# Kernel optimization log

Measured on AMD Instinct MI355X. Metric: run time of the kernel, lower is better.

The kernel has to match this reference:

```python
import jax, jax.numpy as jnp
import numpy as np
from jax import lax

NUM_SKETCH = 3
BN_EPS = 1e-5


def setup_inputs() -> dict:
    key = jax.random.key(0)
    ks = jax.random.split(key, 8)
    B, C, H, W = 32, 128, 64, 64
    D = C // 4  # comp_rate = 4
    k = 3
    x = jax.random.normal(ks[0], (B, C, H, W), dtype=jnp.float32)
    fan = C * k * k
    w1 = jax.random.normal(ks[1], (C, C, k, k), dtype=jnp.float32) / np.sqrt(fan)
    w2 = jax.random.normal(ks[2], (C, C, k, k), dtype=jnp.float32) / np.sqrt(fan)
    gamma1 = jnp.ones((C,), jnp.float32); beta1 = jnp.zeros((C,), jnp.float32)
    gamma2 = jnp.ones((C,), jnp.float32); beta2 = jnp.zeros((C,), jnp.float32)
    # count-sketch hash matrices: hs[j] is (D, C), each column c has a single 1
    idx = jax.random.randint(ks[3], (NUM_SKETCH, C), 0, D)
    hs = jax.nn.one_hot(idx, D, dtype=jnp.float32).transpose(0, 2, 1)  # (3, D, C)
    ss = (jax.random.randint(ks[4], (NUM_SKETCH, C), 0, 2) * 2 - 1).astype(jnp.float32)  # (3, C) signs
    return {"x": x, "w1": w1, "w2": w2, "gamma1": gamma1, "beta1": beta1,
            "gamma2": gamma2, "beta2": beta2, "hs": hs, "ss": ss}


def _sketch_conv_unsketch(x, w, hs, ss):
    # w: (Co, Ci, k, k); hs: (J, D, Co); ss: (J, Co)
    Co, Ci, k, _ = w.shape
    J, D, _ = hs.shape
    B, _, H, W = x.shape
    wf = w.reshape(Co, -1)  # (Co, M)
    # sketched weights per sketch j: h_j @ (wf * s_j[:, None])
    w_sk = jnp.einsum('jdc,jc,cm->jdm', hs, ss, wf).reshape(J * D, Ci, k, k)
    # one conv with J*D output channels (padding=1, stride=1 hardcoded in source)
    y = lax.conv_general_dilated(x, w_sk, window_strides=(1, 1),
                                 padding=[(1, 1), (1, 1)],
                                 dimension_numbers=('NCHW', 'OIHW', 'NCHW'))
    y = y.reshape(B, J, D, H, W)
    # unsketch activations: h_j^T @ y_j, then sign scale (num_s=1 so inner median is identity)
    y_un = jnp.einsum('jdc,bjdhw->jbchw', hs, y) * ss[:, None, :, None, None]
    return jnp.median(y_un, axis=0)  # median over the 3 sketches -> (B, Co, H, W)


def _bn_relu(y, gamma, beta):
    # BatchNorm2d in training mode: biased batch stats over (N, H, W)
    mean = jnp.mean(y, axis=(0, 2, 3), keepdims=True)
    var = jnp.var(y, axis=(0, 2, 3), keepdims=True)
    yhat = (y - mean) * lax.rsqrt(var + BN_EPS)
    return jax.nn.relu(yhat * gamma[None, :, None, None] + beta[None, :, None, None])


def reference(x, w1, w2, gamma1, beta1, gamma2, beta2, hs, ss):
    residual = x
    out1 = _bn_relu(_sketch_conv_unsketch(x, w1, hs, ss), gamma1, beta1)
    del out1  # faithful to source bug: second conv loop uses x, discarding out1
    out = _bn_relu(_sketch_conv_unsketch(x, w2, hs, ss), gamma2, beta2)
    return out + residual
```

## Files before the change

### kernel.cpp

```cpp
#include <hip/hip_runtime.h>
#include <stdint.h>

typedef __bf16 bf16x8 __attribute__((ext_vector_type(8)));
typedef float  f32x4  __attribute__((ext_vector_type(4)));

static constexpr int Bn = 32, Cn = 128, Hn = 64, Wn = 64, HWn = 4096;
static constexpr size_t OFF_XT    = 0;
static constexpr size_t OFF_WF    = 33554432;
static constexpr size_t OFF_IDX   = 33775616;
static constexpr size_t OFF_M     = 33777152;
static constexpr size_t OFF_STATS = 67331584;
static constexpr size_t OFF_ZERO  = 67347968;

__device__ __forceinline__ unsigned short f32_to_bf16(float f) {
    union { float f; unsigned u; } v; v.f = f;
    unsigned u = v.u;
    return (unsigned short)((u + 0x7FFFu + ((u >> 16) & 1u)) >> 16);
}
__device__ __forceinline__ float bf16_to_f32(unsigned short h) {
    union { unsigned u; float f; } v; v.u = ((unsigned)h) << 16;
    return v.f;
}
__device__ __forceinline__ float bf_lo(unsigned w) {
    union { unsigned u; float f; } v; v.u = w << 16; return v.f;
}
__device__ __forceinline__ float bf_hi(unsigned w) {
    union { unsigned u; float f; } v; v.u = w & 0xffff0000u; return v.f;
}
__device__ __forceinline__ float med3(float z0, float z1, float z2) {
    float lo = fminf(z0, z1), hi = fmaxf(z0, z1);
    return fmaxf(lo, fminf(hi, z2));
}
__device__ __forceinline__ void gload_lds16(const unsigned short* g, unsigned short* l) {
    __builtin_amdgcn_global_load_lds(
        (const __attribute__((address_space(1))) unsigned int*)(const void*)g,
        (__attribute__((address_space(3))) unsigned int*)(void*)l,
        16, 0, 0);
}

__global__ __launch_bounds__(256) void k_prep(const float* __restrict__ x,
                                              unsigned short* __restrict__ xT,
                                              const float* __restrict__ w2,
                                              const float* __restrict__ hs,
                                              const float* __restrict__ ss,
                                              unsigned short* __restrict__ wf,
                                              int* __restrict__ idx,
                                              float* __restrict__ stats16,
                                              float* __restrict__ zerop) {
    __shared__ __align__(16) unsigned char smraw[20480];
    int t = threadIdx.x;
    if (blockIdx.x < 432) {
        int*   idxs = (int*)smraw;
        float* sss  = (float*)(smraw + 1536);
        for (int i = t; i < 384; i += 256) {
            int j = i >> 7, c = i & 127;
            int found = 0;
#pragma unroll
            for (int d = 0; d < 32; ++d)
                if (hs[(j * 32 + d) * 128 + c] > 0.5f) found = d;
            idxs[i] = found;
            sss[i]  = ss[i];
        }
        __syncthreads();
        int f = blockIdx.x * 256 + t;
        int jj   = f & 7;
        int lane = (f >> 3) & 63;
        int nt   = (f >> 9) % 6;
        int qt   = f / (512 * 6);
        int tp   = qt % 9;
        int q    = qt / 9;
        int k  = ((lane >> 4) << 3) + jj;
        int ci = q * 32 + k;
        int n  = nt * 16 + (lane & 15);
        int j = n >> 5, d = n & 31;
        const int*   ij = idxs + j * 128;
        const float* sj = sss  + j * 128;
        float sum = 0.f;
        for (int c = 0; c < 128; ++c)
            if (ij[c] == d) sum += sj[c] * w2[(c * 128 + ci) * 9 + tp];
        wf[f] = f32_to_bf16(sum);
    } else if (blockIdx.x == 432) {
        for (int i = t; i < 384; i += 256) {
            int j = i >> 7, c = i & 127;
            int found = 0;
            for (int d = 0; d < 32; ++d)
                if (hs[(j * 32 + d) * 128 + c] > 0.5f) found = d;
            idx[i] = found;
        }
        for (int i = t; i < 4096; i += 256) stats16[i] = 0.f;
        if (t < 32) zerop[t] = 0.f;
    } else {
        unsigned short* sm = (unsigned short*)smraw;
        int blk = blockIdx.x - 433;
        int pt = blk & 15, q = (blk >> 4) & 3, b = blk >> 6;
        int p0 = pt * 256;
        const float* xp = x + ((size_t)(b * Cn + q * 32) * HWn) + p0 + t;
#pragma unroll
        for (int cil = 0; cil < 32; ++cil)
            sm[t * 40 + cil] = f32_to_bf16(xp[(size_t)cil * HWn]);
        __syncthreads();
        uint4* dst = (uint4*)(xT + ((size_t)(b * 4 + q) * HWn + p0) * 32);
#pragma unroll
        for (int pass = 0; pass < 4; ++pass) {
            int pix = pass * 64 + (t >> 2);
            int ch  = t & 3;
            dst[pix * 4 + ch] = *(const uint4*)(&sm[pix * 40 + ch * 8]);
        }
    }
}

__global__ __launch_bounds__(256, 2) void k_conv(const unsigned short* __restrict__ xT,
                                                 const unsigned short* __restrict__ wf,
                                                 const int* __restrict__ idx,
                                                 const float* __restrict__ ss,
                                                 unsigned short* __restrict__ m_out,
                                                 float* __restrict__ stats16,
                                                 const unsigned short* __restrict__ zerop) {
    __shared__ __align__(16) unsigned short sm[25344];
    int tid  = threadIdx.x;
    int blk  = blockIdx.x;
    int tile = blk & 15, b = blk >> 4;
    int ty0  = tile * 4;
    int wv   = tid >> 6, lane = tid & 63;
    int quad = lane >> 4, l15 = lane & 15;

    unsigned short* priv = sm + wv * 6336;

    f32x4 acc[4][6];
#pragma unroll
    for (int a = 0; a < 4; ++a)
#pragma unroll
        for (int nb = 0; nb < 6; ++nb) acc[a][nb] = (f32x4){0.f, 0.f, 0.f, 0.f};

    const unsigned short* wl = wf + lane * 8;

#define STAGE_W(qv)                                                                   \
    {                                                                                 \
        const unsigned short* xq = xT + (size_t)(b * 4 + (qv)) * (HWn * 32);          \
        _Pragma("unroll")                                                             \
        for (int i = 0; i < 13; ++i) {                                                \
            if (i < 12 || lane < 24) {                                                \
                int k  = i * 64 + lane;                                               \
                int r  = k >> 2;                                                      \
                int cl = (k & 3) ^ ((r >> 1) & 3);                                    \
                int dyl = r / 66, hx = r - dyl * 66;                                  \
                int gy = ty0 + wv + dyl - 1, gx = hx - 1;                             \
                const unsigned short* src =                                           \
                    (gy >= 0 && gy < 64 && gx >= 0 && gx < 64)                        \
                        ? (xq + ((gy * 64 + gx) * 32 + cl * 8)) : zerop;              \
                gload_lds16(src, priv + i * 512);                                     \
            }                                                                         \
        }                                                                             \
    }

    STAGE_W(0)
    asm volatile("s_waitcnt vmcnt(0)" ::: "memory");

    for (int q = 0; q < 4; ++q) {
#pragma unroll
        for (int tp = 0; tp < 9; ++tp) {
            int dy = tp / 3, dx = tp % 3;
            bf16x8 bfr[6];
            const unsigned short* wb = wl + (size_t)((q * 9 + tp) * 6) * 512;
#pragma unroll
            for (int nb = 0; nb < 6; ++nb)
                bfr[nb] = *(const bf16x8*)(wb + nb * 512);
            bf16x8 afr[4];
#pragma unroll
            for (int mq = 0; mq < 4; ++mq) {
                int byo = ((dy * 66) + mq * 16 + l15 + dx) * 64 + quad * 16;
                byo ^= ((byo >> 7) & 3) << 4;
                afr[mq] = *(const bf16x8*)((const unsigned char*)priv + byo);
            }
            __builtin_amdgcn_s_setprio(1);
#pragma unroll
            for (int mq = 0; mq < 4; ++mq)
#pragma unroll
                for (int nb = 0; nb < 6; ++nb)
                    acc[mq][nb] = __builtin_amdgcn_mfma_f32_16x16x32_bf16(afr[mq], bfr[nb], acc[mq][nb], 0, 0, 0);
            __builtin_amdgcn_s_setprio(0);
        }
        if (q < 3) {
            STAGE_W(q + 1)
            asm volatile("s_waitcnt vmcnt(0)" ::: "memory");
        }
    }
#undef STAGE_W

    __syncthreads();
#pragma unroll
    for (int mq = 0; mq < 4; ++mq)
#pragma unroll
        for (int nb = 0; nb < 6; ++nb) {
            int ch = nb * 16 + l15;
            int px = wv * 64 + mq * 16 + quad * 4;
            ushort4 v;
            v.x = f32_to_bf16(acc[mq][nb][0]);
            v.y = f32_to_bf16(acc[mq][nb][1]);
            v.z = f32_to_bf16(acc[mq][nb][2]);
            v.w = f32_to_bf16(acc[mq][nb][3]);
            *(ushort4*)(&sm[ch * 264 + px]) = v;
        }
    __syncthreads();
    int half = lane >> 5, p8 = lane & 31;
    unsigned short* mpb = m_out + (size_t)b * Cn * HWn + tile * 256 + p8 * 8;
    float* stp = stats16 + (blk & 15) * 256;
#pragma unroll 2
    for (int i = 0; i < 16; ++i) {
        int c = wv * 32 + i * 2 + half;
        int r0 = idx[c], r1 = 32 + idx[128 + c], r2 = 64 + idx[256 + c];
        float sg0 = ss[c], sg1 = ss[128 + c], sg2 = ss[256 + c];
        uint4 w0 = *(const uint4*)(&sm[r0 * 264 + p8 * 8]);
        uint4 w1 = *(const uint4*)(&sm[r1 * 264 + p8 * 8]);
        uint4 w2v = *(const uint4*)(&sm[r2 * 264 + p8 * 8]);
        const unsigned* u0 = (const unsigned*)&w0;
        const unsigned* u1 = (const unsigned*)&w1;
        const unsigned* u2 = (const unsigned*)&w2v;
        uint4 R;
        unsigned* rw = (unsigned*)&R;
        float s = 0.f, s2 = 0.f;
#pragma unroll
        for (int e = 0; e < 4; ++e) {
            float mlo = med3(sg0 * bf_lo(u0[e]), sg1 * bf_lo(u1[e]), sg2 * bf_lo(u2[e]));
            float mhi = med3(sg0 * bf_hi(u0[e]), sg1 * bf_hi(u1[e]), sg2 * bf_hi(u2[e]));
            s  += mlo + mhi;
            s2 += mlo * mlo + mhi * mhi;
            rw[e] = (unsigned)f32_to_bf16(mlo) | ((unsigned)f32_to_bf16(mhi) << 16);
        }
        *(uint4*)(mpb + (size_t)c * HWn) = R;
#pragma unroll
        for (int o = 16; o > 0; o >>= 1) { s += __shfl_xor(s, o); s2 += __shfl_xor(s2, o); }
        if ((lane & 31) == 0) { atomicAdd(&stp[c], s); atomicAdd(&stp[128 + c], s2); }
    }
}

__global__ __launch_bounds__(256) void k_apply(const unsigned short* __restrict__ m,
                                               const float* __restrict__ x,
                                               const float* __restrict__ stats16,
                                               const float* __restrict__ gamma,
                                               const float* __restrict__ beta,
                                               float* __restrict__ out) {
    __shared__ float co[2];
    int tid = threadIdx.x;
    int i4 = blockIdx.x * 256 + tid;
    int c = (blockIdx.x >> 2) & 127;
    if (tid < 32) {
        float v = stats16[(tid & 15) * 256 + ((tid >> 4) << 7) + c];
#pragma unroll
        for (int o = 8; o > 0; o >>= 1) v += __shfl_xor(v, o);
        if ((tid & 15) == 0) co[tid >> 4] = v;
    }
    __syncthreads();
    const float N = 131072.f;
    float mean = co[0] / N;
    float var  = co[1] / N - mean * mean;
    float sc   = gamma[c] * rsqrtf(var + 1e-5f);
    float sh   = beta[c] - mean * sc;
    ushort4 mv = ((const ushort4*)m)[i4];
    float4  xv = ((const float4*)x)[i4];
    float4 o;
    o.x = fmaxf(bf16_to_f32(mv.x) * sc + sh, 0.f) + xv.x;
    o.y = fmaxf(bf16_to_f32(mv.y) * sc + sh, 0.f) + xv.y;
    o.z = fmaxf(bf16_to_f32(mv.z) * sc + sh, 0.f) + xv.z;
    o.w = fmaxf(bf16_to_f32(mv.w) * sc + sh, 0.f) + xv.w;
    ((float4*)out)[i4] = o;
}

extern "C" void kernel_launch(void* const* d_in, const int* in_sizes, int n_in,
                              void* d_out, int out_size, void* d_ws, size_t ws_size,
                              hipStream_t stream) {
    const float* x      = (const float*)d_in[0];
    const float* w2     = (const float*)d_in[2];
    const float* gamma2 = (const float*)d_in[5];
    const float* beta2  = (const float*)d_in[6];
    const float* hs     = (const float*)d_in[7];
    const float* ss     = (const float*)d_in[8];
    float* out = (float*)d_out;

    char* ws = (char*)d_ws;
    unsigned short* xT  = (unsigned short*)(ws + OFF_XT);
    unsigned short* wfp = (unsigned short*)(ws + OFF_WF);
    int*            idp = (int*)(ws + OFF_IDX);
    unsigned short* mp  = (unsigned short*)(ws + OFF_M);
    float*          st  = (float*)(ws + OFF_STATS);
    float*          zp  = (float*)(ws + OFF_ZERO);

    k_prep<<<2481, 256, 0, stream>>>(x, xT, w2, hs, ss, wfp, idp, st, zp);
    k_conv<<<512, 256, 0, stream>>>(xT, wfp, idp, ss, mp, st, (const unsigned short*)zp);
    k_apply<<<16384, 256, 0, stream>>>(mp, x, st, gamma2, beta2, out);
}
```

Measured before the change: 197.3 us.

## Restructure conv tiling: full-channel halo staged once, waves split rows and output channels

The transposed input layout becomes pixel-major with all 128 channels contiguous, so each conv block stages its whole 2-row halo for all channels into LDS in one pass instead of re-staging per 32-channel quarter with a blocking wait. Blocks now cover 2 output rows and 1024 blocks are launched; each wave handles one row and half of the 96 sketched output channels, which halves its accumulator count. Stats buffers grow to 32 partial slots. This removes the serialized per-quarter load stalls and lowers register pressure, at the cost of more LDS per block, more blocks, and duplicated weight fragment loads across waves.

```diff
diff --git a/kernel.cpp b/kernel.cpp
--- a/kernel.cpp
+++ b/kernel.cpp
@@ -10,7 +10,7 @@
 static constexpr size_t OFF_IDX   = 33775616;
 static constexpr size_t OFF_M     = 33777152;
 static constexpr size_t OFF_STATS = 67331584;
-static constexpr size_t OFF_ZERO  = 67347968;
+static constexpr size_t OFF_ZERO  = 67364352;
 
 __device__ __forceinline__ unsigned short f32_to_bf16(float f) {
     union { float f; unsigned u; } v; v.f = f;
@@ -45,7 +45,7 @@
                                               const float* __restrict__ ss,
                                               unsigned short* __restrict__ wf,
                                               int* __restrict__ idx,
-                                              float* __restrict__ stats16,
+                                              float* __restrict__ stats32,
                                               float* __restrict__ zerop) {
     __shared__ __align__(16) unsigned char smraw[20480];
     int t = threadIdx.x;
@@ -87,8 +87,8 @@
                 if (hs[(j * 32 + d) * 128 + c] > 0.5f) found = d;
             idx[i] = found;
         }
-        for (int i = t; i < 4096; i += 256) stats16[i] = 0.f;
-        if (t < 32) zerop[t] = 0.f;
+        for (int i = t; i < 8192; i += 256) stats32[i] = 0.f;
+        if (t < 64) zerop[t] = 0.f;
     } else {
         unsigned short* sm = (unsigned short*)smraw;
         int blk = blockIdx.x - 433;
@@ -99,12 +99,12 @@
         for (int cil = 0; cil < 32; ++cil)
             sm[t * 40 + cil] = f32_to_bf16(xp[(size_t)cil * HWn]);
         __syncthreads();
-        uint4* dst = (uint4*)(xT + ((size_t)(b * 4 + q) * HWn + p0) * 32);
+        uint4* dst = (uint4*)xT;
 #pragma unroll
         for (int pass = 0; pass < 4; ++pass) {
             int pix = pass * 64 + (t >> 2);
             int ch  = t & 3;
-            dst[pix * 4 + ch] = *(const uint4*)(&sm[pix * 40 + ch * 8]);
+            dst[(size_t)(b * HWn + p0 + pix) * 16 + q * 4 + ch] = *(const uint4*)(&sm[pix * 40 + ch * 8]);
         }
     }
 }
@@ -114,105 +114,93 @@
                                                  const int* __restrict__ idx,
                                                  const float* __restrict__ ss,
                                                  unsigned short* __restrict__ m_out,
-                                                 float* __restrict__ stats16,
+                                                 float* __restrict__ stats32,
                                                  const unsigned short* __restrict__ zerop) {
-    __shared__ __align__(16) unsigned short sm[25344];
+    __shared__ __align__(16) unsigned short sm[33792];
     int tid  = threadIdx.x;
     int blk  = blockIdx.x;
-    int tile = blk & 15, b = blk >> 4;
-    int ty0  = tile * 4;
+    int tile = blk & 31, b = blk >> 5;
+    int ty0  = tile * 2;
     int wv   = tid >> 6, lane = tid & 63;
     int quad = lane >> 4, l15 = lane & 15;
-
-    unsigned short* priv = sm + wv * 6336;
-
-    f32x4 acc[4][6];
+    int row_l = wv >> 1, nh = wv & 1;
+
+    {
+        const unsigned short* xb = xT + (size_t)b * (HWn * 128);
+#pragma unroll
+        for (int i = 0; i < 17; ++i) {
+            if (i < 16 || tid < 128) {
+                int k  = i * 256 + tid;
+                int r  = k >> 4, cl = k & 15;
+                int sl = cl ^ (r & 7);
+                int hy = r / 66, hx = r - hy * 66;
+                int gy = ty0 + hy - 1, gx = hx - 1;
+                const unsigned short* src = (gy >= 0 && gy < 64 && gx >= 0 && gx < 64)
+                        ? (xb + ((size_t)(gy * 64 + gx) * 128 + sl * 8)) : zerop;
+                gload_lds16(src, &sm[(size_t)k * 8]);
+            }
+        }
+    }
+    __syncthreads();
+
+    f32x4 acc[4][3];
 #pragma unroll
     for (int a = 0; a < 4; ++a)
 #pragma unroll
-        for (int nb = 0; nb < 6; ++nb) acc[a][nb] = (f32x4){0.f, 0.f, 0.f, 0.f};
-
-    const unsigned short* wl = wf + lane * 8;
-
-#define STAGE_W(qv)                                                                   \
-    {                                                                                 \
-        const unsigned short* xq = xT + (size_t)(b * 4 + (qv)) * (HWn * 32);          \
-        _Pragma("unroll")                                                             \
-        for (int i = 0; i < 13; ++i) {                                                \
-            if (i < 12 || lane < 24) {                                                \
-                int k  = i * 64 + lane;                                               \
-                int r  = k >> 2;                                                      \
-                int cl = (k & 3) ^ ((r >> 1) & 3);                                    \
-                int dyl = r / 66, hx = r - dyl * 66;                                  \
-                int gy = ty0 + wv + dyl - 1, gx = hx - 1;                             \
-                const unsigned short* src =                                           \
-                    (gy >= 0 && gy < 64 && gx >= 0 && gx < 64)                        \
-                        ? (xq + ((gy * 64 + gx) * 32 + cl * 8)) : zerop;              \
-                gload_lds16(src, priv + i * 512);                                     \
-            }                                                                         \
-        }                                                                             \
-    }
-
-    STAGE_W(0)
-    asm volatile("s_waitcnt vmcnt(0)" ::: "memory");
+        for (int nb = 0; nb < 3; ++nb) acc[a][nb] = (f32x4){0.f, 0.f, 0.f, 0.f};
+
+    const unsigned short* wl = wf + (size_t)(nh * 3) * 512 + lane * 8;
 
     for (int q = 0; q < 4; ++q) {
 #pragma unroll
         for (int tp = 0; tp < 9; ++tp) {
             int dy = tp / 3, dx = tp % 3;
-            bf16x8 bfr[6];
+            bf16x8 bfr[3];
             const unsigned short* wb = wl + (size_t)((q * 9 + tp) * 6) * 512;
 #pragma unroll
-            for (int nb = 0; nb < 6; ++nb)
+            for (int nb = 0; nb < 3; ++nb)
                 bfr[nb] = *(const bf16x8*)(wb + nb * 512);
+            int rb = (row_l + dy) * 66 + l15 + dx;
+            int sw = ((4 * q + quad) ^ (rb & 7)) * 16;
             bf16x8 afr[4];
 #pragma unroll
-            for (int mq = 0; mq < 4; ++mq) {
-                int byo = ((dy * 66) + mq * 16 + l15 + dx) * 64 + quad * 16;
-                byo ^= ((byo >> 7) & 3) << 4;
-                afr[mq] = *(const bf16x8*)((const unsigned char*)priv + byo);
-            }
+            for (int mq = 0; mq < 4; ++mq)
+                afr[mq] = *(const bf16x8*)((const unsigned char*)sm + (rb + mq * 16) * 256 + sw);
             __builtin_amdgcn_s_setprio(1);
 #pragma unroll
             for (int mq = 0; mq < 4; ++mq)
 #pragma unroll
-                for (int nb = 0; nb < 6; ++nb)
+                for (int nb = 0; nb < 3; ++nb)
                     acc[mq][nb] = __builtin_amdgcn_mfma_f32_16x16x32_bf16(afr[mq], bfr[nb], acc[mq][nb], 0, 0, 0);
             __builtin_amdgcn_s_setprio(0);
         }
-        if (q < 3) {
-            STAGE_W(q + 1)
-            asm volatile("s_waitcnt vmcnt(0)" ::: "memory");
-        }
-    }
-#undef STAGE_W
+    }
 
     __syncthreads();
 #pragma unroll
     for (int mq = 0; mq < 4; ++mq)
 #pragma unroll
-        for (int nb = 0; nb < 6; ++nb) {
-            int ch = nb * 16 + l15;
-            int px = wv * 64 + mq * 16 + quad * 4;
+        for (int nb = 0; nb < 3; ++nb) {
+            int ch = nh * 48 + nb * 16 + l15;
+            int px = row_l * 64 + mq * 16 + quad * 4;
             ushort4 v;
             v.x = f32_to_bf16(acc[mq][nb][0]);
             v.y = f32_to_bf16(acc[mq][nb][1]);
             v.z = f32_to_bf16(acc[mq][nb][2]);
             v.w = f32_to_bf16(acc[mq][nb][3]);
-            *(ushort4*)(&sm[ch * 264 + px]) = v;
-        }
-    __syncthreads();
-    int half = lane >> 5, p8 = lane & 31;
-    unsigned short* mpb = m_out + (size_t)b * Cn * HWn + tile * 256 + p8 * 8;
-    float* stp = stats16 + (blk & 15) * 256;
+            *(ushort4*)(&sm[ch * 136 + px]) = v;
+        }
+    __syncthreads();
+    unsigned short* mpb = m_out + (size_t)b * Cn * HWn + tile * 128 + l15 * 8;
+    float* stp = stats32 + (blk & 31) * 256;
 #pragma unroll 2
-    for (int i = 0; i < 16; ++i) {
-        int c = wv * 32 + i * 2 + half;
+    for (int i = 0; i < 8; ++i) {
+        int c = wv * 32 + i * 4 + quad;
         int r0 = idx[c], r1 = 32 + idx[128 + c], r2 = 64 + idx[256 + c];
         float sg0 = ss[c], sg1 = ss[128 + c], sg2 = ss[256 + c];
-        uint4 w0 = *(const uint4*)(&sm[r0 * 264 + p8 * 8]);
-        uint4 w1 = *(const uint4*)(&sm[r1 * 264 + p8 * 8]);
-        uint4 w2v = *(const uint4*)(&sm[r2 * 264 + p8 * 8]);
+        uint4 w0 = *(const uint4*)(&sm[r0 * 136 + l15 * 8]);
+        uint4 w1 = *(const uint4*)(&sm[r1 * 136 + l15 * 8]);
+        uint4 w2v = *(const uint4*)(&sm[r2 * 136 + l15 * 8]);
         const unsigned* u0 = (const unsigned*)&w0;
         const unsigned* u1 = (const unsigned*)&w1;
         const unsigned* u2 = (const unsigned*)&w2v;
@@ -229,14 +217,14 @@
         }
         *(uint4*)(mpb + (size_t)c * HWn) = R;
 #pragma unroll
-        for (int o = 16; o > 0; o >>= 1) { s += __shfl_xor(s, o); s2 += __shfl_xor(s2, o); }
-        if ((lane & 31) == 0) { atomicAdd(&stp[c], s); atomicAdd(&stp[128 + c], s2); }
+        for (int o = 8; o > 0; o >>= 1) { s += __shfl_xor(s, o); s2 += __shfl_xor(s2, o); }
+        if (l15 == 0) { atomicAdd(&stp[c], s); atomicAdd(&stp[128 + c], s2); }
     }
 }
 
 __global__ __launch_bounds__(256) void k_apply(const unsigned short* __restrict__ m,
                                                const float* __restrict__ x,
-                                               const float* __restrict__ stats16,
+                                               const float* __restrict__ stats32,
                                                const float* __restrict__ gamma,
                                                const float* __restrict__ beta,
                                                float* __restrict__ out) {
@@ -244,11 +232,11 @@
     int tid = threadIdx.x;
     int i4 = blockIdx.x * 256 + tid;
     int c = (blockIdx.x >> 2) & 127;
-    if (tid < 32) {
-        float v = stats16[(tid & 15) * 256 + ((tid >> 4) << 7) + c];
-#pragma unroll
-        for (int o = 8; o > 0; o >>= 1) v += __shfl_xor(v, o);
-        if ((tid & 15) == 0) co[tid >> 4] = v;
+    if (tid < 64) {
+        float v = stats32[(tid & 31) * 256 + ((tid >> 5) << 7) + c];
+#pragma unroll
+        for (int o = 16; o > 0; o >>= 1) v += __shfl_xor(v, o);
+        if ((tid & 31) == 0) co[tid >> 5] = v;
     }
     __syncthreads();
     const float N = 131072.f;
@@ -286,6 +274,6 @@
     float*          zp  = (float*)(ws + OFF_ZERO);
 
     k_prep<<<2481, 256, 0, stream>>>(x, xT, w2, hs, ss, wfp, idp, st, zp);
-    k_conv<<<512, 256, 0, stream>>>(xT, wfp, idp, ss, mp, st, (const unsigned short*)zp);
+    k_conv<<<1024, 256, 0, stream>>>(xT, wfp, idp, ss, mp, st, (const unsigned short*)zp);
     k_apply<<<16384, 256, 0, stream>>>(mp, x, st, gamma2, beta2, out);
 }
```

After: 209.7 us. 1.06x slower.
